# Kernel tuning notes

Measured on AMD Instinct MI355X. Metric: run time of the kernel, lower is better.

Reference implementation:

```python
import jax, jax.numpy as jnp
import numpy as np

N = 50000      # nodes
E = 800000     # edges (avg degree 16)
F_IN = 512
HID = 128
OUT = 64
NIDX = 1000


def setup_inputs() -> dict:
    key = jax.random.key(0)
    ks = jax.random.split(key, 7)
    x = jax.random.normal(ks[0], (N, F_IN), dtype=jnp.float32)
    edge_src = jax.random.randint(ks[1], (E,), 0, N)
    edge_dst = jax.random.randint(ks[2], (E,), 0, N)
    edge_weight = jax.random.uniform(ks[3], (E,), dtype=jnp.float32)
    W0 = jax.random.normal(ks[4], (F_IN, HID), dtype=jnp.float32) * (1.0 / np.sqrt(F_IN))
    W1 = jax.random.normal(ks[5], (HID, OUT), dtype=jnp.float32) * (1.0 / np.sqrt(HID))
    idx = jax.random.randint(ks[6], (NIDX,), 0, N)
    return {"x": x, "W0": W0, "W1": W1, "edge_weight": edge_weight,
            "edge_src": edge_src, "edge_dst": edge_dst, "idx": idx}


def _spmm(edge_src, edge_dst, edge_weight, h):
    # sparse adj @ h in COO form: gather rows by src, weight, scatter-add to dst
    msg = h[edge_src] * edge_weight[:, None]          # [E, d]
    return jax.ops.segment_sum(msg, edge_dst, num_segments=N)  # [N, d]


def reference(x, W0, W1, edge_weight, edge_src, edge_dst, idx):
    # layer 0: GraphConvolution (x @ W then adj spmm), relu; dropout omitted (eval)
    h = jax.nn.relu(_spmm(edge_src, edge_dst, edge_weight, x @ W0))  # [N, HID]
    # layer 1: final GraphConvolution, no activation
    out = _spmm(edge_src, edge_dst, edge_weight, h @ W1)             # [N, OUT]
    return out[idx]                                                  # [NIDX, OUT]
```

## Files before the change

### kernel.cpp

```cpp
#include <hip/hip_runtime.h>
#include <hip/hip_bf16.h>

#define N_NODES 50000
#define F_IN    512
#define HID     128
#define OUT_F   64
#define NIDX    1000
#define E_NUM   800000
#define CAP     48
#define MAXFLAG 20480
#define NSCAN2  196

typedef __attribute__((ext_vector_type(8))) short short8;
typedef __attribute__((ext_vector_type(4))) float f32x4;

__device__ inline ushort f2bf(float f) {
    __hip_bfloat16 h = __float2bfloat16(f);
    return *reinterpret_cast<ushort*>(&h);
}
__device__ inline float bf2f(ushort u) {
    return __uint_as_float(((uint)u) << 16);
}
__device__ inline short8 pack8(f32x4 a, f32x4 b) {
    short8 r;
    r[0] = (short)f2bf(a[0]); r[1] = (short)f2bf(a[1]);
    r[2] = (short)f2bf(a[2]); r[3] = (short)f2bf(a[3]);
    r[4] = (short)f2bf(b[0]); r[5] = (short)f2bf(b[1]);
    r[6] = (short)f2bf(b[2]); r[7] = (short)f2bf(b[3]);
    return r;
}

#define GLOAD_LDS16(g, l) __builtin_amdgcn_global_load_lds( \
    (const __attribute__((address_space(1))) unsigned int*)(g), \
    (__attribute__((address_space(3))) unsigned int*)(l), 16, 0, 0)

__global__ __launch_bounds__(256) void prep_kernel(const float* __restrict__ W0,
                                                   ushort* __restrict__ W0t,
                                                   const int* __restrict__ idx,
                                                   ushort* __restrict__ jmap) {
    const int b = blockIdx.x;
    if (b < 64) {
        __shared__ float tl[32][33];
        const int k0 = (b & 15) * 32, n0 = (b >> 4) * 32;
        const int tx = threadIdx.x & 31, ty = threadIdx.x >> 5;
#pragma unroll
        for (int i = 0; i < 4; ++i)
            tl[ty + i * 8][tx] = W0[(size_t)(k0 + ty + i * 8) * HID + n0 + tx];
        __syncthreads();
#pragma unroll
        for (int i = 0; i < 4; ++i) {
            const int n = ty + i * 8;
            W0t[(size_t)(n0 + n) * F_IN + k0 + tx] = f2bf(tl[tx][n]);
        }
    } else {
        const int j = (b - 64) * 256 + threadIdx.x;
        if (j < NIDX) jmap[idx[j]] = (ushort)(j + 1);
    }
}

__global__ __launch_bounds__(256, 3) void fused_gemm_scan2(
        const float* __restrict__ x, const ushort* __restrict__ W0t,
        ushort* __restrict__ XW0b,
        const int* __restrict__ esrc, const int* __restrict__ edst,
        const float* __restrict__ ew, const ushort* __restrict__ flags,
        int* __restrict__ countsB, int2* __restrict__ bktB) {
    __shared__ __align__(16) char smem[49152];

    if (blockIdx.x < NSCAN2) {
        const int tid = blockIdx.x * 256 + threadIdx.x;
        for (int q = tid; q < E_NUM / 4; q += NSCAN2 * 256) {
            const int e0 = q * 4;
            const int4   d4 = *(const int4*)(edst + e0);
            const int4   s4 = *(const int4*)(esrc + e0);
            const float4 w4 = *(const float4*)(ew + e0);
#define DOIT(DD, SS, WW) { const int s = flags[DD]; if (s) { \
        const int c = atomicAdd(&countsB[s - 1], 1); \
        if (c < CAP) bktB[(size_t)(s - 1) * CAP + c] = make_int2(SS, __float_as_int(WW)); } }
            DOIT(d4.x, s4.x, w4.x) DOIT(d4.y, s4.y, w4.y)
            DOIT(d4.z, s4.z, w4.z) DOIT(d4.w, s4.w, w4.w)
#undef DOIT
        }
        return;
    }

    const int t = threadIdx.x;
    const int w = t >> 6, lane = t & 63;
    const int wr = w >> 1, wc = w & 1;
    const int lr = lane & 15, lk = lane >> 4;
    const int m0 = (blockIdx.x - NSCAN2) * 64;

    f32x4 acc[2][4] = {};

    auto stage = [&](int buf, int k0) {
        char* lA = smem + buf * 8192;
        char* lB = smem + 24576 + buf * 8192;
#pragma unroll
        for (int i = 0; i < 2; ++i) {
            {
                const int o = i * 256 + t;
                const int row = o >> 3, c = o & 7;
                int grow = m0 + row; if (grow > N_NODES - 1) grow = N_NODES - 1;
                const float* g = x + (size_t)grow * F_IN + k0 + ((c ^ (row & 7)) << 2);
                GLOAD_LDS16(g, lA + (i * 256 + w * 64) * 16);
            }
            {
                const int o = i * 256 + t;
                const int row = o >> 2, c = o & 3;
                const ushort* g = W0t + (size_t)row * F_IN + k0 + ((c ^ ((row >> 1) & 3)) << 3);
                GLOAD_LDS16(g, lB + (i * 256 + w * 64) * 16);
            }
        }
    };

    stage(0, 0);
    stage(1, 32);
    stage(2, 64);
#pragma unroll
    for (int kt = 0; kt < 16; ++kt) {
        const int rem = 15 - kt;
        if (rem >= 2)      asm volatile("s_waitcnt vmcnt(8)" ::: "memory");
        else if (rem == 1) asm volatile("s_waitcnt vmcnt(4)" ::: "memory");
        else               asm volatile("s_waitcnt vmcnt(0)" ::: "memory");
        __builtin_amdgcn_s_barrier();

        const int cur = kt % 3;
        const float*  Af = (const float*)(smem + cur * 8192);
        const ushort* Bf = (const ushort*)(smem + 24576 + cur * 8192);
        short8 a[2], b[4];
#pragma unroll
        for (int mi = 0; mi < 2; ++mi) {
            const int R = wr * 32 + mi * 16 + lr;
            const float* ar = Af + R * 32;
            const f32x4 lo = *(const f32x4*)(ar + (((2 * lk + 0) ^ (R & 7)) << 2));
            const f32x4 hi = *(const f32x4*)(ar + (((2 * lk + 1) ^ (R & 7)) << 2));
            a[mi] = pack8(lo, hi);
        }
#pragma unroll
        for (int ni = 0; ni < 4; ++ni) {
            const int n = wc * 64 + ni * 16 + lr;
            b[ni] = *(const short8*)(Bf + n * 32 + ((lk ^ ((n >> 1) & 3)) << 3));
        }
        asm volatile("s_waitcnt lgkmcnt(0)" ::: "memory");
        __builtin_amdgcn_s_barrier();

        if (kt <= 12) stage(cur, (kt + 3) * 32);

#pragma unroll
        for (int mi = 0; mi < 2; ++mi)
#pragma unroll
            for (int ni = 0; ni < 4; ++ni)
                acc[mi][ni] = __builtin_amdgcn_mfma_f32_16x16x32_bf16(
                    a[mi], b[ni], acc[mi][ni], 0, 0, 0);
    }

    float* ep = (float*)smem + w * (16 * 68);
#pragma unroll
    for (int mi = 0; mi < 2; ++mi) {
        __syncthreads();
#pragma unroll
        for (int ni = 0; ni < 4; ++ni)
#pragma unroll
            for (int r = 0; r < 4; ++r)
                ep[(lk * 4 + r) * 68 + ni * 16 + lr] = acc[mi][ni][r];
        __syncthreads();
        const int rr = lane >> 2, cq = lane & 3;
        const int grow = m0 + wr * 32 + mi * 16 + rr;
        alignas(16) float vv[16];
#pragma unroll
        for (int j = 0; j < 4; ++j)
            *(f32x4*)&vv[j * 4] = *(const f32x4*)&ep[rr * 68 + cq * 16 + j * 4];
        if (grow < N_NODES) {
            alignas(16) ushort us[16];
#pragma unroll
            for (int jj = 0; jj < 16; ++jj) us[jj] = f2bf(vv[jj]);
            ushort* orow = XW0b + (size_t)grow * HID + wc * 64 + cq * 16;
            *(uint4*)(orow)     = *(const uint4*)&us[0];
            *(uint4*)(orow + 8) = *(const uint4*)&us[8];
        }
    }
}

__global__ __launch_bounds__(256) void bucket_idx_kernel(const int* __restrict__ esrc,
                                                         const int* __restrict__ edst,
                                                         const float* __restrict__ ew,
                                                         const ushort* __restrict__ jmap,
                                                         int* __restrict__ countsA,
                                                         int2* __restrict__ bktA,
                                                         ushort* __restrict__ flags) {
    const int e0 = (blockIdx.x * 256 + threadIdx.x) * 4;
    if (e0 >= E_NUM) return;
    const int4   d4 = *(const int4*)(edst + e0);
    const int4   s4 = *(const int4*)(esrc + e0);
    const float4 w4 = *(const float4*)(ew + e0);
#define DOIT(DD, SS, WW) { const int rep = jmap[DD]; if (rep) { \
        const int r = rep - 1; const int c = atomicAdd(&countsA[r], 1); \
        if (c < CAP) bktA[(size_t)r * CAP + c] = make_int2(SS, __float_as_int(WW)); \
        flags[SS] = 1; } }
    DOIT(d4.x, s4.x, w4.x) DOIT(d4.y, s4.y, w4.y)
    DOIT(d4.z, s4.z, w4.z) DOIT(d4.w, s4.w, w4.w)
#undef DOIT
}

__global__ __launch_bounds__(256) void compact_kernel(ushort* __restrict__ flags,
                                                      int* __restrict__ list,
                                                      int* __restrict__ nflag) {
    const int n = blockIdx.x * 256 + threadIdx.x;
    if (n < N_NODES && flags[n]) {
        const int s = atomicAdd(nflag, 1);
        if (s < MAXFLAG) { flags[n] = (ushort)(s + 1); list[s] = n; }
        else flags[n] = 0;
    }
}

__global__ __launch_bounds__(256) void spmm1_kernel(const ushort* __restrict__ XW0b,
                                                    const int* __restrict__ list,
                                                    const int* __restrict__ nflag,
                                                    const int* __restrict__ countsB,
                                                    const int2* __restrict__ bktB,
                                                    ushort* __restrict__ H) {
    const int lane = threadIdx.x & 63;
    const int nf = *nflag;
    const int nw = gridDim.x * 4;
    for (int wdx = blockIdx.x * 4 + (threadIdx.x >> 6); wdx < nf; wdx += nw) {
        const int n = list[wdx];
        const int deg = min(countsB[wdx], CAP);
        float a0 = 0.f, a1 = 0.f;
        int c = 0;
        for (; c + 3 < deg; c += 4) {
            const int2 p0 = bktB[(size_t)wdx * CAP + c];
            const int2 p1 = bktB[(size_t)wdx * CAP + c + 1];
            const int2 p2 = bktB[(size_t)wdx * CAP + c + 2];
            const int2 p3 = bktB[(size_t)wdx * CAP + c + 3];
            const uint v0 = *(const uint*)(XW0b + (size_t)p0.x * HID + 2 * lane);
            const uint v1 = *(const uint*)(XW0b + (size_t)p1.x * HID + 2 * lane);
            const uint v2 = *(const uint*)(XW0b + (size_t)p2.x * HID + 2 * lane);
            const uint v3 = *(const uint*)(XW0b + (size_t)p3.x * HID + 2 * lane);
            const float w0 = __int_as_float(p0.y), w1 = __int_as_float(p1.y);
            const float w2 = __int_as_float(p2.y), w3 = __int_as_float(p3.y);
            a0 += w0 * bf2f((ushort)(v0 & 0xffffu)) + w1 * bf2f((ushort)(v1 & 0xffffu))
                + w2 * bf2f((ushort)(v2 & 0xffffu)) + w3 * bf2f((ushort)(v3 & 0xffffu));
            a1 += w0 * bf2f((ushort)(v0 >> 16))     + w1 * bf2f((ushort)(v1 >> 16))
                + w2 * bf2f((ushort)(v2 >> 16))     + w3 * bf2f((ushort)(v3 >> 16));
        }
        for (; c < deg; ++c) {
            const int2 p = bktB[(size_t)wdx * CAP + c];
            const float wt = __int_as_float(p.y);
            const uint v = *(const uint*)(XW0b + (size_t)p.x * HID + 2 * lane);
            a0 += wt * bf2f((ushort)(v & 0xffffu));
            a1 += wt * bf2f((ushort)(v >> 16));
        }
        const uint o = (uint)f2bf(fmaxf(a0, 0.f)) | ((uint)f2bf(fmaxf(a1, 0.f)) << 16);
        *(uint*)(H + (size_t)n * HID + 2 * lane) = o;
    }
}

__global__ __launch_bounds__(64) void spmm2_kernel(const ushort* __restrict__ H,
                                                   const float* __restrict__ W1,
                                                   const int* __restrict__ idx,
                                                   const ushort* __restrict__ jmap,
                                                   const int* __restrict__ countsA,
                                                   const int2* __restrict__ bktA,
                                                   float* __restrict__ outp) {
    __shared__ float aggs[HID];
    const int j = blockIdx.x, lane = threadIdx.x;
    const int r = (int)jmap[idx[j]] - 1;
    const int deg = min(countsA[r], CAP);
    float a0 = 0.f, a1 = 0.f;
    for (int c = 0; c < deg; ++c) {
        const int2 p = bktA[(size_t)r * CAP + c];
        const float wt = __int_as_float(p.y);
        const uint v = *(const uint*)(H + (size_t)p.x * HID + 2 * lane);
        a0 += wt * bf2f((ushort)(v & 0xffffu));
        a1 += wt * bf2f((ushort)(v >> 16));
    }
    aggs[2 * lane] = a0; aggs[2 * lane + 1] = a1;
    __syncthreads();
    float s = 0.f;
#pragma unroll 8
    for (int k = 0; k < HID; ++k) s += aggs[k] * W1[k * OUT_F + lane];
    outp[(size_t)j * OUT_F + lane] = s;
}

extern "C" void kernel_launch(void* const* d_in, const int* in_sizes, int n_in,
                              void* d_out, int out_size, void* d_ws, size_t ws_size,
                              hipStream_t stream) {
    const float* x    = (const float*)d_in[0];
    const float* W0   = (const float*)d_in[1];
    const float* W1   = (const float*)d_in[2];
    const float* ew   = (const float*)d_in[3];
    const int*   esrc = (const int*)d_in[4];
    const int*   edst = (const int*)d_in[5];
    const int*   idx  = (const int*)d_in[6];
    float* outp = (float*)d_out;

    char* ws = (char*)d_ws;
    ushort* XW0b   = (ushort*)(ws);
    ushort* H      = (ushort*)(ws + 12800000);
    ushort* W0t    = (ushort*)(ws + 25600000);
    int2*   bktA   = (int2*)  (ws + 25731072);
    int2*   bktB   = (int2*)  (ws + 26115072);
    int*    list   = (int*)   (ws + 33979392);
    char*   zbase  = ws + 34061312;
    int*    countsA = (int*)   (zbase);
    int*    countsB = (int*)   (zbase + 4096);
    ushort* flags   = (ushort*)(zbase + 86016);
    ushort* jmap    = (ushort*)(zbase + 186368);
    int*    nflag   = (int*)   (zbase + 286720);
    hipMemsetAsync(zbase, 0, 286976, stream);

    prep_kernel       <<<68, 256, 0, stream>>>(W0, W0t, idx, jmap);
    bucket_idx_kernel <<<(E_NUM / 4 + 255) / 256, 256, 0, stream>>>(esrc, edst, ew, jmap, countsA, bktA, flags);
    compact_kernel    <<<(N_NODES + 255) / 256, 256, 0, stream>>>(flags, list, nflag);
    fused_gemm_scan2  <<<NSCAN2 + (N_NODES + 63) / 64, 256, 0, stream>>>(
                          x, W0t, XW0b, esrc, edst, ew, flags, countsB, bktB);
    spmm1_kernel      <<<1024, 256, 0, stream>>>(XW0b, list, nflag, countsB, bktB, H);
    spmm2_kernel      <<<NIDX, 64, 0, stream>>>(H, W1, idx, jmap, countsA, bktA, outp);
}
```

Before: 92.87 us.

## Pre-convert x to bf16 in fused scan kernel and retile GEMM to 128 rows

Adds a kernel that converts x from fp32 to bf16 into a workspace buffer while the first edge-bucketing scan runs in the same launch, replacing the separate bucket_idx kernel. The GEMM now reads bf16 x, uses 128-row tiles with 64-wide K steps and a single LDS buffer with __syncthreads, and drops the triple-buffered async pipeline and swizzles. The aim is to halve GEMM A-operand traffic and raise tile reuse. In exchange it adds a full extra read and write of x and loses load/compute overlap, and the unswizzled LDS reads may hit bank conflicts.

```diff
diff --git a/kernel.cpp b/kernel.cpp
--- a/kernel.cpp
+++ b/kernel.cpp
@@ -9,7 +9,9 @@
 #define E_NUM   800000
 #define CAP     48
 #define MAXFLAG 20480
-#define NSCAN2  196
+#define NSCAN   196
+#define NPREB   1024
+#define NGROUP  3200000
 
 typedef __attribute__((ext_vector_type(8))) short short8;
 typedef __attribute__((ext_vector_type(4))) float f32x4;
@@ -58,17 +60,46 @@
     }
 }
 
-__global__ __launch_bounds__(256, 3) void fused_gemm_scan2(
-        const float* __restrict__ x, const ushort* __restrict__ W0t,
+__global__ __launch_bounds__(256) void fused_pre_scan1(
+        const float* __restrict__ x, ushort* __restrict__ xb,
+        const int* __restrict__ esrc, const int* __restrict__ edst,
+        const float* __restrict__ ew, const ushort* __restrict__ jmap,
+        int* __restrict__ countsA, int2* __restrict__ bktA,
+        ushort* __restrict__ flags) {
+    if (blockIdx.x < NSCAN) {
+        for (int q = blockIdx.x * 256 + threadIdx.x; q < E_NUM / 4; q += NSCAN * 256) {
+            const int e0 = q * 4;
+            const int4   d4 = *(const int4*)(edst + e0);
+            const int4   s4 = *(const int4*)(esrc + e0);
+            const float4 w4 = *(const float4*)(ew + e0);
+#define DOIT(DD, SS, WW) { const int rep = jmap[DD]; if (rep) { \
+        const int r = rep - 1; const int c = atomicAdd(&countsA[r], 1); \
+        if (c < CAP) bktA[(size_t)r * CAP + c] = make_int2(SS, __float_as_int(WW)); \
+        flags[SS] = 1; } }
+            DOIT(d4.x, s4.x, w4.x) DOIT(d4.y, s4.y, w4.y)
+            DOIT(d4.z, s4.z, w4.z) DOIT(d4.w, s4.w, w4.w)
+#undef DOIT
+        }
+        return;
+    }
+    for (int g = (blockIdx.x - NSCAN) * 256 + threadIdx.x; g < NGROUP; g += NPREB * 256) {
+        const f32x4 v0 = *(const f32x4*)(x + (size_t)g * 8);
+        const f32x4 v1 = *(const f32x4*)(x + (size_t)g * 8 + 4);
+        const short8 p = pack8(v0, v1);
+        *(short8*)(xb + (size_t)g * 8) = p;
+    }
+}
+
+__global__ __launch_bounds__(256, 4) void fused_gemm_scan2(
+        const ushort* __restrict__ xb, const ushort* __restrict__ W0t,
         ushort* __restrict__ XW0b,
         const int* __restrict__ esrc, const int* __restrict__ edst,
         const float* __restrict__ ew, const ushort* __restrict__ flags,
         int* __restrict__ countsB, int2* __restrict__ bktB) {
-    __shared__ __align__(16) char smem[49152];
-
-    if (blockIdx.x < NSCAN2) {
-        const int tid = blockIdx.x * 256 + threadIdx.x;
-        for (int q = tid; q < E_NUM / 4; q += NSCAN2 * 256) {
+    __shared__ __align__(16) char smem[32768];
+
+    if (blockIdx.x < NSCAN) {
+        for (int q = blockIdx.x * 256 + threadIdx.x; q < E_NUM / 4; q += NSCAN * 256) {
             const int e0 = q * 4;
             const int4   d4 = *(const int4*)(edst + e0);
             const int4   s4 = *(const int4*)(esrc + e0);
@@ -87,75 +118,47 @@
     const int w = t >> 6, lane = t & 63;
     const int wr = w >> 1, wc = w & 1;
     const int lr = lane & 15, lk = lane >> 4;
-    const int m0 = (blockIdx.x - NSCAN2) * 64;
-
-    f32x4 acc[2][4] = {};
-
-    auto stage = [&](int buf, int k0) {
-        char* lA = smem + buf * 8192;
-        char* lB = smem + 24576 + buf * 8192;
-#pragma unroll
-        for (int i = 0; i < 2; ++i) {
-            {
-                const int o = i * 256 + t;
-                const int row = o >> 3, c = o & 7;
-                int grow = m0 + row; if (grow > N_NODES - 1) grow = N_NODES - 1;
-                const float* g = x + (size_t)grow * F_IN + k0 + ((c ^ (row & 7)) << 2);
-                GLOAD_LDS16(g, lA + (i * 256 + w * 64) * 16);
-            }
-            {
-                const int o = i * 256 + t;
-                const int row = o >> 2, c = o & 3;
-                const ushort* g = W0t + (size_t)row * F_IN + k0 + ((c ^ ((row >> 1) & 3)) << 3);
-                GLOAD_LDS16(g, lB + (i * 256 + w * 64) * 16);
-            }
-        }
-    };
-
-    stage(0, 0);
-    stage(1, 32);
-    stage(2, 64);
-#pragma unroll
-    for (int kt = 0; kt < 16; ++kt) {
-        const int rem = 15 - kt;
-        if (rem >= 2)      asm volatile("s_waitcnt vmcnt(8)" ::: "memory");
-        else if (rem == 1) asm volatile("s_waitcnt vmcnt(4)" ::: "memory");
-        else               asm volatile("s_waitcnt vmcnt(0)" ::: "memory");
-        __builtin_amdgcn_s_barrier();
-
-        const int cur = kt % 3;
-        const float*  Af = (const float*)(smem + cur * 8192);
-        const ushort* Bf = (const ushort*)(smem + 24576 + cur * 8192);
-        short8 a[2], b[4];
-#pragma unroll
-        for (int mi = 0; mi < 2; ++mi) {
-            const int R = wr * 32 + mi * 16 + lr;
-            const float* ar = Af + R * 32;
-            const f32x4 lo = *(const f32x4*)(ar + (((2 * lk + 0) ^ (R & 7)) << 2));
-            const f32x4 hi = *(const f32x4*)(ar + (((2 * lk + 1) ^ (R & 7)) << 2));
-            a[mi] = pack8(lo, hi);
-        }
-#pragma unroll
-        for (int ni = 0; ni < 4; ++ni) {
-            const int n = wc * 64 + ni * 16 + lr;
-            b[ni] = *(const short8*)(Bf + n * 32 + ((lk ^ ((n >> 1) & 3)) << 3));
-        }
-        asm volatile("s_waitcnt lgkmcnt(0)" ::: "memory");
-        __builtin_amdgcn_s_barrier();
-
-        if (kt <= 12) stage(cur, (kt + 3) * 32);
-
-#pragma unroll
-        for (int mi = 0; mi < 2; ++mi)
+    const int m0 = (blockIdx.x - NSCAN) * 128;
+
+    char* lA = smem;
+    char* lB = smem + 16384;
+    f32x4 acc[4][4] = {};
+
+    for (int kt = 0; kt < 8; ++kt) {
+        const int k0 = kt * 64;
+#pragma unroll
+        for (int i = 0; i < 4; ++i) {
+            const int o = i * 256 + t;
+            const int row = o >> 3, c = o & 7;
+            int ga = m0 + row; if (ga > N_NODES - 1) ga = N_NODES - 1;
+            GLOAD_LDS16(xb + (size_t)ga * F_IN + k0 + c * 8, lA + (i * 256 + w * 64) * 16);
+            GLOAD_LDS16(W0t + (size_t)row * F_IN + k0 + c * 8, lB + (i * 256 + w * 64) * 16);
+        }
+        __syncthreads();
+
+#pragma unroll
+        for (int kk = 0; kk < 2; ++kk) {
+            const int kb = kk * 64 + lk * 16;
+            short8 a[4], b[4];
+#pragma unroll
+            for (int mi = 0; mi < 4; ++mi)
+                a[mi] = *(const short8*)(lA + (wr * 64 + mi * 16 + lr) * 128 + kb);
 #pragma unroll
             for (int ni = 0; ni < 4; ++ni)
-                acc[mi][ni] = __builtin_amdgcn_mfma_f32_16x16x32_bf16(
-                    a[mi], b[ni], acc[mi][ni], 0, 0, 0);
+                b[ni] = *(const short8*)(lB + (wc * 64 + ni * 16 + lr) * 128 + kb);
+#pragma unroll
+            for (int mi = 0; mi < 4; ++mi)
+#pragma unroll
+                for (int ni = 0; ni < 4; ++ni)
+                    acc[mi][ni] = __builtin_amdgcn_mfma_f32_16x16x32_bf16(
+                        a[mi], b[ni], acc[mi][ni], 0, 0, 0);
+        }
+        __syncthreads();
     }
 
     float* ep = (float*)smem + w * (16 * 68);
 #pragma unroll
-    for (int mi = 0; mi < 2; ++mi) {
+    for (int mi = 0; mi < 4; ++mi) {
         __syncthreads();
 #pragma unroll
         for (int ni = 0; ni < 4; ++ni)
@@ -164,7 +167,7 @@
                 ep[(lk * 4 + r) * 68 + ni * 16 + lr] = acc[mi][ni][r];
         __syncthreads();
         const int rr = lane >> 2, cq = lane & 3;
-        const int grow = m0 + wr * 32 + mi * 16 + rr;
+        const int grow = m0 + wr * 64 + mi * 16 + rr;
         alignas(16) float vv[16];
 #pragma unroll
         for (int j = 0; j < 4; ++j)
@@ -178,27 +181,6 @@
             *(uint4*)(orow + 8) = *(const uint4*)&us[8];
         }
     }
-}
-
-__global__ __launch_bounds__(256) void bucket_idx_kernel(const int* __restrict__ esrc,
-                                                         const int* __restrict__ edst,
-                                                         const float* __restrict__ ew,
-                                                         const ushort* __restrict__ jmap,
-                                                         int* __restrict__ countsA,
-                                                         int2* __restrict__ bktA,
-                                                         ushort* __restrict__ flags) {
-    const int e0 = (blockIdx.x * 256 + threadIdx.x) * 4;
-    if (e0 >= E_NUM) return;
-    const int4   d4 = *(const int4*)(edst + e0);
-    const int4   s4 = *(const int4*)(esrc + e0);
-    const float4 w4 = *(const float4*)(ew + e0);
-#define DOIT(DD, SS, WW) { const int rep = jmap[DD]; if (rep) { \
-        const int r = rep - 1; const int c = atomicAdd(&countsA[r], 1); \
-        if (c < CAP) bktA[(size_t)r * CAP + c] = make_int2(SS, __float_as_int(WW)); \
-        flags[SS] = 1; } }
-    DOIT(d4.x, s4.x, w4.x) DOIT(d4.y, s4.y, w4.y)
-    DOIT(d4.z, s4.z, w4.z) DOIT(d4.w, s4.w, w4.w)
-#undef DOIT
 }
 
 __global__ __launch_bounds__(256) void compact_kernel(ushort* __restrict__ flags,
@@ -306,13 +288,15 @@
     ushort* flags   = (ushort*)(zbase + 86016);
     ushort* jmap    = (ushort*)(zbase + 186368);
     int*    nflag   = (int*)   (zbase + 286720);
+    ushort* xb      = (ushort*)(ws + 34348288);
     hipMemsetAsync(zbase, 0, 286976, stream);
 
-    prep_kernel       <<<68, 256, 0, stream>>>(W0, W0t, idx, jmap);
-    bucket_idx_kernel <<<(E_NUM / 4 + 255) / 256, 256, 0, stream>>>(esrc, edst, ew, jmap, countsA, bktA, flags);
-    compact_kernel    <<<(N_NODES + 255) / 256, 256, 0, stream>>>(flags, list, nflag);
-    fused_gemm_scan2  <<<NSCAN2 + (N_NODES + 63) / 64, 256, 0, stream>>>(
-                          x, W0t, XW0b, esrc, edst, ew, flags, countsB, bktB);
-    spmm1_kernel      <<<1024, 256, 0, stream>>>(XW0b, list, nflag, countsB, bktB, H);
-    spmm2_kernel      <<<NIDX, 64, 0, stream>>>(H, W1, idx, jmap, countsA, bktA, outp);
-}
+    prep_kernel    <<<68, 256, 0, stream>>>(W0, W0t, idx, jmap);
+    fused_pre_scan1<<<NSCAN + NPREB, 256, 0, stream>>>(x, xb, esrc, edst, ew, jmap,
+                                                       countsA, bktA, flags);
+    compact_kernel <<<(N_NODES + 255) / 256, 256, 0, stream>>>(flags, list, nflag);
+    fused_gemm_scan2<<<NSCAN + (N_NODES + 127) / 128, 256, 0, stream>>>(
+                        xb, W0t, XW0b, esrc, edst, ew, flags, countsB, bktB);
+    spmm1_kernel   <<<1024, 256, 0, stream>>>(XW0b, list, nflag, countsB, bktB, H);
+    spmm2_kernel   <<<NIDX, 64, 0, stream>>>(H, W1, idx, jmap, countsA, bktA, outp);
+}
```

Result: slower. 107.2 us (+15.5%).

## Restructure x@W0 GEMM to single-wave 32-row blocks reading W0t from global

Applied to the files above, without the earlier changes.

Rewrites the fused GEMM part to use 64-thread single-wave blocks, each computing a 32x128 output tile. Only x is staged through LDS, now double-buffered, while the bf16 W0t fragments are loaded directly from global memory (expected to stay in L2/cache) on every k-step. This cuts LDS use and block-level barriers and allows higher occupancy, at the cost of more global/L2 traffic for W0t and less intra-block reuse. The scan portion now also runs with 64 threads per block, so it has fewer scanning threads in total.

```diff
diff --git a/kernel.cpp b/kernel.cpp
--- a/kernel.cpp
+++ b/kernel.cpp
@@ -9,7 +9,8 @@
 #define E_NUM   800000
 #define CAP     48
 #define MAXFLAG 20480
-#define NSCAN2  196
+#define NSCAN   196
+#define NGBLK   1563
 
 typedef __attribute__((ext_vector_type(8))) short short8;
 typedef __attribute__((ext_vector_type(4))) float f32x4;
@@ -58,17 +59,16 @@
     }
 }
 
-__global__ __launch_bounds__(256, 3) void fused_gemm_scan2(
+__global__ __launch_bounds__(64, 3) void fused_gemm_scan2(
         const float* __restrict__ x, const ushort* __restrict__ W0t,
         ushort* __restrict__ XW0b,
         const int* __restrict__ esrc, const int* __restrict__ edst,
         const float* __restrict__ ew, const ushort* __restrict__ flags,
         int* __restrict__ countsB, int2* __restrict__ bktB) {
-    __shared__ __align__(16) char smem[49152];
-
-    if (blockIdx.x < NSCAN2) {
-        const int tid = blockIdx.x * 256 + threadIdx.x;
-        for (int q = tid; q < E_NUM / 4; q += NSCAN2 * 256) {
+    __shared__ __align__(16) char smem[8704];
+
+    if (blockIdx.x < NSCAN) {
+        for (int q = blockIdx.x * 64 + threadIdx.x; q < E_NUM / 4; q += NSCAN * 64) {
             const int e0 = q * 4;
             const int4   d4 = *(const int4*)(edst + e0);
             const int4   s4 = *(const int4*)(esrc + e0);
@@ -83,99 +83,79 @@
         return;
     }
 
-    const int t = threadIdx.x;
-    const int w = t >> 6, lane = t & 63;
-    const int wr = w >> 1, wc = w & 1;
+    const int lane = threadIdx.x;
     const int lr = lane & 15, lk = lane >> 4;
-    const int m0 = (blockIdx.x - NSCAN2) * 64;
-
-    f32x4 acc[2][4] = {};
-
-    auto stage = [&](int buf, int k0) {
-        char* lA = smem + buf * 8192;
-        char* lB = smem + 24576 + buf * 8192;
-#pragma unroll
-        for (int i = 0; i < 2; ++i) {
-            {
-                const int o = i * 256 + t;
-                const int row = o >> 3, c = o & 7;
-                int grow = m0 + row; if (grow > N_NODES - 1) grow = N_NODES - 1;
-                const float* g = x + (size_t)grow * F_IN + k0 + ((c ^ (row & 7)) << 2);
-                GLOAD_LDS16(g, lA + (i * 256 + w * 64) * 16);
-            }
-            {
-                const int o = i * 256 + t;
-                const int row = o >> 2, c = o & 3;
-                const ushort* g = W0t + (size_t)row * F_IN + k0 + ((c ^ ((row >> 1) & 3)) << 3);
-                GLOAD_LDS16(g, lB + (i * 256 + w * 64) * 16);
-            }
+    const int m0 = (blockIdx.x - NSCAN) * 32;
+
+    f32x4 acc[2][8] = {};
+
+    auto stage = [&](int buf, int kt) {
+#pragma unroll
+        for (int j = 0; j < 4; ++j) {
+            const int c = j * 64 + lane;
+            const int r = c >> 3;
+            int grow = m0 + r; if (grow > N_NODES - 1) grow = N_NODES - 1;
+            const float* g = x + (size_t)grow * F_IN + kt * 32 + (((c & 7) ^ (r & 7)) << 2);
+            GLOAD_LDS16(g, smem + buf * 4096 + j * 1024);
         }
     };
 
     stage(0, 0);
-    stage(1, 32);
-    stage(2, 64);
+    stage(1, 1);
+    const ushort* wbase = W0t + (size_t)lr * F_IN + lk * 8;
 #pragma unroll
     for (int kt = 0; kt < 16; ++kt) {
-        const int rem = 15 - kt;
-        if (rem >= 2)      asm volatile("s_waitcnt vmcnt(8)" ::: "memory");
-        else if (rem == 1) asm volatile("s_waitcnt vmcnt(4)" ::: "memory");
-        else               asm volatile("s_waitcnt vmcnt(0)" ::: "memory");
-        __builtin_amdgcn_s_barrier();
-
-        const int cur = kt % 3;
-        const float*  Af = (const float*)(smem + cur * 8192);
-        const ushort* Bf = (const ushort*)(smem + 24576 + cur * 8192);
-        short8 a[2], b[4];
-#pragma unroll
-        for (int mi = 0; mi < 2; ++mi) {
-            const int R = wr * 32 + mi * 16 + lr;
-            const float* ar = Af + R * 32;
-            const f32x4 lo = *(const f32x4*)(ar + (((2 * lk + 0) ^ (R & 7)) << 2));
-            const f32x4 hi = *(const f32x4*)(ar + (((2 * lk + 1) ^ (R & 7)) << 2));
-            a[mi] = pack8(lo, hi);
-        }
-#pragma unroll
-        for (int ni = 0; ni < 4; ++ni) {
-            const int n = wc * 64 + ni * 16 + lr;
-            b[ni] = *(const short8*)(Bf + n * 32 + ((lk ^ ((n >> 1) & 3)) << 3));
-        }
-        asm volatile("s_waitcnt lgkmcnt(0)" ::: "memory");
-        __builtin_amdgcn_s_barrier();
-
-        if (kt <= 12) stage(cur, (kt + 3) * 32);
-
-#pragma unroll
-        for (int mi = 0; mi < 2; ++mi)
-#pragma unroll
-            for (int ni = 0; ni < 4; ++ni)
-                acc[mi][ni] = __builtin_amdgcn_mfma_f32_16x16x32_bf16(
-                    a[mi], b[ni], acc[mi][ni], 0, 0, 0);
-    }
-
-    float* ep = (float*)smem + w * (16 * 68);
+        short8 b[8];
+#pragma unroll
+        for (int ni = 0; ni < 8; ++ni)
+            b[ni] = *(const short8*)(wbase + (size_t)ni * 16 * F_IN + kt * 32);
+        if (kt < 15) asm volatile("s_waitcnt vmcnt(12)" ::: "memory");
+        else         asm volatile("s_waitcnt vmcnt(8)" ::: "memory");
+
+        const char* Ab = smem + (kt & 1) * 4096;
+        const int ch0 = (((2 * lk) ^ (lr & 7)) << 4);
+        const int ch1 = (((2 * lk + 1) ^ (lr & 7)) << 4);
+        const f32x4 lo0 = *(const f32x4*)(Ab + lr * 128 + ch0);
+        const f32x4 hi0 = *(const f32x4*)(Ab + lr * 128 + ch1);
+        const f32x4 lo1 = *(const f32x4*)(Ab + (16 + lr) * 128 + ch0);
+        const f32x4 hi1 = *(const f32x4*)(Ab + (16 + lr) * 128 + ch1);
+        const short8 a0 = pack8(lo0, hi0);
+        const short8 a1 = pack8(lo1, hi1);
+
+        if (kt < 14) stage(kt & 1, kt + 2);
+
+#pragma unroll
+        for (int ni = 0; ni < 8; ++ni) {
+            acc[0][ni] = __builtin_amdgcn_mfma_f32_16x16x32_bf16(a0, b[ni], acc[0][ni], 0, 0, 0);
+            acc[1][ni] = __builtin_amdgcn_mfma_f32_16x16x32_bf16(a1, b[ni], acc[1][ni], 0, 0, 0);
+        }
+    }
+    __syncthreads();
+
+    float* ep = (float*)smem;
 #pragma unroll
     for (int mi = 0; mi < 2; ++mi) {
         __syncthreads();
 #pragma unroll
-        for (int ni = 0; ni < 4; ++ni)
+        for (int ni = 0; ni < 8; ++ni)
 #pragma unroll
             for (int r = 0; r < 4; ++r)
-                ep[(lk * 4 + r) * 68 + ni * 16 + lr] = acc[mi][ni][r];
+                ep[(lk * 4 + r) * 136 + ni * 16 + lr] = acc[mi][ni][r];
         __syncthreads();
-        const int rr = lane >> 2, cq = lane & 3;
-        const int grow = m0 + wr * 32 + mi * 16 + rr;
-        alignas(16) float vv[16];
-#pragma unroll
-        for (int j = 0; j < 4; ++j)
-            *(f32x4*)&vv[j * 4] = *(const f32x4*)&ep[rr * 68 + cq * 16 + j * 4];
+        const int rr = lane >> 2, cg = lane & 3;
+        const int grow = m0 + mi * 16 + rr;
+        alignas(16) float vv[32];
+#pragma unroll
+        for (int j = 0; j < 8; ++j)
+            *(f32x4*)&vv[j * 4] = *(const f32x4*)&ep[rr * 136 + cg * 32 + j * 4];
         if (grow < N_NODES) {
-            alignas(16) ushort us[16];
-#pragma unroll
-            for (int jj = 0; jj < 16; ++jj) us[jj] = f2bf(vv[jj]);
-            ushort* orow = XW0b + (size_t)grow * HID + wc * 64 + cq * 16;
-            *(uint4*)(orow)     = *(const uint4*)&us[0];
-            *(uint4*)(orow + 8) = *(const uint4*)&us[8];
+            alignas(16) ushort us[32];
+#pragma unroll
+            for (int jj = 0; jj < 32; ++jj) us[jj] = f2bf(vv[jj]);
+            ushort* orow = XW0b + (size_t)grow * HID + cg * 32;
+#pragma unroll
+            for (int k = 0; k < 4; ++k)
+                *(uint4*)(orow + k * 8) = *(const uint4*)&us[k * 8];
         }
     }
 }
@@ -308,11 +288,11 @@
     int*    nflag   = (int*)   (zbase + 286720);
     hipMemsetAsync(zbase, 0, 286976, stream);
 
-    prep_kernel       <<<68, 256, 0, stream>>>(W0, W0t, idx, jmap);
-    bucket_idx_kernel <<<(E_NUM / 4 + 255) / 256, 256, 0, stream>>>(esrc, edst, ew, jmap, countsA, bktA, flags);
-    compact_kernel    <<<(N_NODES + 255) / 256, 256, 0, stream>>>(flags, list, nflag);
-    fused_gemm_scan2  <<<NSCAN2 + (N_NODES + 63) / 64, 256, 0, stream>>>(
-                          x, W0t, XW0b, esrc, edst, ew, flags, countsB, bktB);
-    spmm1_kernel      <<<1024, 256, 0, stream>>>(XW0b, list, nflag, countsB, bktB, H);
-    spmm2_kernel      <<<NIDX, 64, 0, stream>>>(H, W1, idx, jmap, countsA, bktA, outp);
-}
+    prep_kernel      <<<68, 256, 0, stream>>>(W0, W0t, idx, jmap);
+    bucket_idx_kernel<<<(E_NUM / 4 + 255) / 256, 256, 0, stream>>>(esrc, edst, ew, jmap, countsA, bktA, flags);
+    compact_kernel   <<<(N_NODES + 255) / 256, 256, 0, stream>>>(flags, list, nflag);
+    fused_gemm_scan2 <<<NSCAN + NGBLK, 64, 0, stream>>>(
+                         x, W0t, XW0b, esrc, edst, ew, flags, countsB, bktB);
+    spmm1_kernel     <<<1024, 256, 0, stream>>>(XW0b, list, nflag, countsB, bktB, H);
+    spmm2_kernel     <<<NIDX, 64, 0, stream>>>(H, W1, idx, jmap, countsA, bktA, outp);
+}
```

Measured after the change: 126.6 us. 1.36x slower.

## Replace triple-buffered async GEMM pipeline with single-buffer BK=64 loop for higher occupancy

Applied to the files above, without the earlier changes.

The x@W0 GEMM part of the fused kernel drops its 3-stage software pipeline (BK=32, 48KB LDS, explicit vmcnt waits) in favour of one 32KB buffer with BK=64 and plain syncthreads around each tile. Launch bounds go from 3 to 5 blocks per CU. The aim is to hide memory latency through more resident waves instead of in-block prefetching. The cost is that loads are no longer overlapped with MFMA inside a block, and each k-step now takes two barriers.

```diff
diff --git a/kernel.cpp b/kernel.cpp
--- a/kernel.cpp
+++ b/kernel.cpp
@@ -9,7 +9,8 @@
 #define E_NUM   800000
 #define CAP     48
 #define MAXFLAG 20480
-#define NSCAN2  196
+#define NSCAN   196
+#define NGBLK   782
 
 typedef __attribute__((ext_vector_type(8))) short short8;
 typedef __attribute__((ext_vector_type(4))) float f32x4;
@@ -58,17 +59,16 @@
     }
 }
 
-__global__ __launch_bounds__(256, 3) void fused_gemm_scan2(
+__global__ __launch_bounds__(256, 5) void fused_gemm_scan2(
         const float* __restrict__ x, const ushort* __restrict__ W0t,
         ushort* __restrict__ XW0b,
         const int* __restrict__ esrc, const int* __restrict__ edst,
         const float* __restrict__ ew, const ushort* __restrict__ flags,
         int* __restrict__ countsB, int2* __restrict__ bktB) {
-    __shared__ __align__(16) char smem[49152];
-
-    if (blockIdx.x < NSCAN2) {
-        const int tid = blockIdx.x * 256 + threadIdx.x;
-        for (int q = tid; q < E_NUM / 4; q += NSCAN2 * 256) {
+    __shared__ __align__(16) char smem[32768];
+
+    if (blockIdx.x < NSCAN) {
+        for (int q = blockIdx.x * 256 + threadIdx.x; q < E_NUM / 4; q += NSCAN * 256) {
             const int e0 = q * 4;
             const int4   d4 = *(const int4*)(edst + e0);
             const int4   s4 = *(const int4*)(esrc + e0);
@@ -87,70 +87,56 @@
     const int w = t >> 6, lane = t & 63;
     const int wr = w >> 1, wc = w & 1;
     const int lr = lane & 15, lk = lane >> 4;
-    const int m0 = (blockIdx.x - NSCAN2) * 64;
-
+    const int m0 = (blockIdx.x - NSCAN) * 64;
+
+    char* lA = smem;
+    char* lB = smem + 16384;
     f32x4 acc[2][4] = {};
 
-    auto stage = [&](int buf, int k0) {
-        char* lA = smem + buf * 8192;
-        char* lB = smem + 24576 + buf * 8192;
-#pragma unroll
-        for (int i = 0; i < 2; ++i) {
+    for (int kt = 0; kt < 8; ++kt) {
+        const int k0 = kt * 64;
+#pragma unroll
+        for (int i = 0; i < 4; ++i) {
+            const int o = i * 256 + t;
             {
-                const int o = i * 256 + t;
-                const int row = o >> 3, c = o & 7;
-                int grow = m0 + row; if (grow > N_NODES - 1) grow = N_NODES - 1;
-                const float* g = x + (size_t)grow * F_IN + k0 + ((c ^ (row & 7)) << 2);
+                const int row = o >> 4, c = o & 15;
+                int ga = m0 + row; if (ga > N_NODES - 1) ga = N_NODES - 1;
+                const float* g = x + (size_t)ga * F_IN + k0 + ((c ^ ((row & 7) << 1)) << 2);
                 GLOAD_LDS16(g, lA + (i * 256 + w * 64) * 16);
             }
             {
-                const int o = i * 256 + t;
-                const int row = o >> 2, c = o & 3;
-                const ushort* g = W0t + (size_t)row * F_IN + k0 + ((c ^ ((row >> 1) & 3)) << 3);
+                const int row = o >> 3, c = o & 7;
+                const ushort* g = W0t + (size_t)row * F_IN + k0 + ((c ^ (row & 7)) << 3);
                 GLOAD_LDS16(g, lB + (i * 256 + w * 64) * 16);
             }
         }
-    };
-
-    stage(0, 0);
-    stage(1, 32);
-    stage(2, 64);
-#pragma unroll
-    for (int kt = 0; kt < 16; ++kt) {
-        const int rem = 15 - kt;
-        if (rem >= 2)      asm volatile("s_waitcnt vmcnt(8)" ::: "memory");
-        else if (rem == 1) asm volatile("s_waitcnt vmcnt(4)" ::: "memory");
-        else               asm volatile("s_waitcnt vmcnt(0)" ::: "memory");
-        __builtin_amdgcn_s_barrier();
-
-        const int cur = kt % 3;
-        const float*  Af = (const float*)(smem + cur * 8192);
-        const ushort* Bf = (const ushort*)(smem + 24576 + cur * 8192);
-        short8 a[2], b[4];
-#pragma unroll
-        for (int mi = 0; mi < 2; ++mi) {
-            const int R = wr * 32 + mi * 16 + lr;
-            const float* ar = Af + R * 32;
-            const f32x4 lo = *(const f32x4*)(ar + (((2 * lk + 0) ^ (R & 7)) << 2));
-            const f32x4 hi = *(const f32x4*)(ar + (((2 * lk + 1) ^ (R & 7)) << 2));
-            a[mi] = pack8(lo, hi);
-        }
-#pragma unroll
-        for (int ni = 0; ni < 4; ++ni) {
-            const int n = wc * 64 + ni * 16 + lr;
-            b[ni] = *(const short8*)(Bf + n * 32 + ((lk ^ ((n >> 1) & 3)) << 3));
-        }
-        asm volatile("s_waitcnt lgkmcnt(0)" ::: "memory");
-        __builtin_amdgcn_s_barrier();
-
-        if (kt <= 12) stage(cur, (kt + 3) * 32);
-
-#pragma unroll
-        for (int mi = 0; mi < 2; ++mi)
-#pragma unroll
-            for (int ni = 0; ni < 4; ++ni)
-                acc[mi][ni] = __builtin_amdgcn_mfma_f32_16x16x32_bf16(
-                    a[mi], b[ni], acc[mi][ni], 0, 0, 0);
+        __syncthreads();
+
+#pragma unroll
+        for (int kk = 0; kk < 2; ++kk) {
+            short8 a[2], b[4];
+#pragma unroll
+            for (int mi = 0; mi < 2; ++mi) {
+                const int R = wr * 32 + mi * 16 + lr;
+                const int cs = (kk * 8 + lk * 2) ^ ((R & 7) << 1);
+                const f32x4 lo = *(const f32x4*)(lA + R * 256 + (cs << 4));
+                const f32x4 hi = *(const f32x4*)(lA + R * 256 + (cs << 4) + 16);
+                a[mi] = pack8(lo, hi);
+            }
+#pragma unroll
+            for (int ni = 0; ni < 4; ++ni) {
+                const int Rb = wc * 64 + ni * 16 + lr;
+                const int cs = (kk * 4 + lk) ^ (Rb & 7);
+                b[ni] = *(const short8*)(lB + Rb * 128 + (cs << 4));
+            }
+#pragma unroll
+            for (int mi = 0; mi < 2; ++mi)
+#pragma unroll
+                for (int ni = 0; ni < 4; ++ni)
+                    acc[mi][ni] = __builtin_amdgcn_mfma_f32_16x16x32_bf16(
+                        a[mi], b[ni], acc[mi][ni], 0, 0, 0);
+        }
+        __syncthreads();
     }
 
     float* ep = (float*)smem + w * (16 * 68);
@@ -308,11 +294,11 @@
     int*    nflag   = (int*)   (zbase + 286720);
     hipMemsetAsync(zbase, 0, 286976, stream);
 
-    prep_kernel       <<<68, 256, 0, stream>>>(W0, W0t, idx, jmap);
-    bucket_idx_kernel <<<(E_NUM / 4 + 255) / 256, 256, 0, stream>>>(esrc, edst, ew, jmap, countsA, bktA, flags);
-    compact_kernel    <<<(N_NODES + 255) / 256, 256, 0, stream>>>(flags, list, nflag);
-    fused_gemm_scan2  <<<NSCAN2 + (N_NODES + 63) / 64, 256, 0, stream>>>(
-                          x, W0t, XW0b, esrc, edst, ew, flags, countsB, bktB);
-    spmm1_kernel      <<<1024, 256, 0, stream>>>(XW0b, list, nflag, countsB, bktB, H);
-    spmm2_kernel      <<<NIDX, 64, 0, stream>>>(H, W1, idx, jmap, countsA, bktA, outp);
-}
+    prep_kernel      <<<68, 256, 0, stream>>>(W0, W0t, idx, jmap);
+    bucket_idx_kernel<<<(E_NUM / 4 + 255) / 256, 256, 0, stream>>>(esrc, edst, ew, jmap, countsA, bktA, flags);
+    compact_kernel   <<<(N_NODES + 255) / 256, 256, 0, stream>>>(flags, list, nflag);
+    fused_gemm_scan2 <<<NSCAN + NGBLK, 256, 0, stream>>>(
+                         x, W0t, XW0b, esrc, edst, ew, flags, countsB, bktB);
+    spmm1_kernel     <<<1024, 256, 0, stream>>>(XW0b, list, nflag, countsB, bktB, H);
+    spmm2_kernel     <<<NIDX, 64, 0, stream>>>(H, W1, idx, jmap, countsA, bktA, outp);
+}
```

Result: no change. 91.74 us (-1.2%).
